# Kernel tuning notes

Hardware: AMD Instinct MI355X
Metric: run time of the kernel (lower is better)

The kernel has to match this reference:

```python
import jax, jax.numpy as jnp
import numpy as np

VOCAB, EMBED, CTX, HID = 32000, 512, 512, 1024
BATCH, MAX_LEN, START = 32, 64, 1


def setup_inputs() -> dict:
    key = jax.random.key(0)
    ks = jax.random.split(key, 12)
    s_emb = 1.0 / np.sqrt(EMBED)
    s_h = 1.0 / np.sqrt(HID)
    inp = {
        "context": jax.random.normal(ks[0], (BATCH, 1, CTX), jnp.float32),
        "max_len": MAX_LEN,
        "emb": jax.random.normal(ks[1], (VOCAB, EMBED), jnp.float32) * s_emb,
        "W_ih0": jax.random.normal(ks[2], (4 * HID, EMBED + CTX), jnp.float32) * s_h,
        "W_hh0": jax.random.normal(ks[3], (4 * HID, HID), jnp.float32) * s_h,
        "b_ih0": jax.random.normal(ks[4], (4 * HID,), jnp.float32) * s_h,
        "b_hh0": jax.random.normal(ks[5], (4 * HID,), jnp.float32) * s_h,
        "W_ih1": jax.random.normal(ks[6], (4 * HID, HID), jnp.float32) * s_h,
        "W_hh1": jax.random.normal(ks[7], (4 * HID, HID), jnp.float32) * s_h,
        "b_ih1": jax.random.normal(ks[8], (4 * HID,), jnp.float32) * s_h,
        "b_hh1": jax.random.normal(ks[9], (4 * HID,), jnp.float32) * s_h,
        "W_lin": jax.random.normal(ks[10], (VOCAB, HID), jnp.float32) * s_h,
        "b_lin": jax.random.normal(ks[11], (VOCAB,), jnp.float32) * s_h,
    }
    return inp


def _lstm_cell(x, h, c, W_ih, W_hh, b_ih, b_hh):
    # PyTorch LSTM gate order: i, f, g, o
    g = x @ W_ih.T + b_ih + h @ W_hh.T + b_hh  # (B, 4H)
    i, f, gg, o = jnp.split(g, 4, axis=-1)
    i, f, o = jax.nn.sigmoid(i), jax.nn.sigmoid(f), jax.nn.sigmoid(o)
    c_new = f * c + i * jnp.tanh(gg)
    h_new = o * jnp.tanh(c_new)
    return h_new, c_new


def reference(context, max_len, emb, W_ih0, W_hh0, b_ih0, b_hh0,
              W_ih1, W_hh1, b_ih1, b_hh1, W_lin, b_lin):
    B = context.shape[0]
    ctx = context[:, 0, :]  # (B, CTX)
    H = W_hh0.shape[1]
    x0 = jnp.full((B,), START, dtype=jnp.int32)
    zeros = jnp.zeros((B, H), jnp.float32)

    def step(carry, _):
        x, h0, c0, h1, c1 = carry
        ex = emb[x]                                   # (B, E) embedding lookup
        inp = jnp.concatenate([ex, ctx], axis=-1)      # (B, E+CTX)
        h0, c0 = _lstm_cell(inp, h0, c0, W_ih0, W_hh0, b_ih0, b_hh0)
        h1, c1 = _lstm_cell(h0, h1, c1, W_ih1, W_hh1, b_ih1, b_hh1)
        probs = jax.nn.softmax(h1 @ W_lin.T + b_lin, axis=-1)  # (B, V)
        x_next = jax.lax.stop_gradient(jnp.argmax(probs, axis=-1).astype(jnp.int32))
        return (x_next, h0, c0, h1, c1), probs

    _, probs_seq = jax.lax.scan(step, (x0, zeros, zeros, zeros, zeros), None, length=max_len)
    return jnp.transpose(probs_seq, (1, 0, 2))  # (B, max_len, V)
```

## Files before the change

### kernel.cpp

```cpp
#include <hip/hip_runtime.h>
#include <math.h>

#define B 32
#define E 512
#define CTXD 512
#define H 1024
#define G4 4096
#define V 32000
#define T 64
#define LDW 1024
#define START_TOK 1

#define OFF_GCTX   0L
#define OFF_H0     131072L
#define OFF_C0     163840L
#define OFF_H1     196608L
#define OFF_C1     229376L
#define OFF_PART0  262144L
#define OFF_PART1  1048576L
#define OFF_BSUM1  2097152L
#define OFF_SUMS   2101248L
#define OFF_AMAX   2103296L

__device__ __forceinline__ void gemm_tile(
    const float* __restrict__ W, int wcol, int j0, int xcol, int klen, int tid,
    const float* const* srow,
    float (&Wt)[64][129], float (&Xs)[32][64], float (&acc)[2][8])
{
  const int jj = tid & 63;
  const int bg = tid >> 6;
  for (int kc = 0; kc < klen; kc += 64) {
#pragma unroll
    for (int i = 0; i < 8; i++) {
      int fi  = tid + (i << 8);
      int row = fi >> 4;
      int c4  = (fi & 15) << 2;
      const float4 w4 = *(const float4*)(W + (long)(j0 + row) * LDW + (wcol + kc + c4));
      Wt[c4 + 0][row] = w4.x;
      Wt[c4 + 1][row] = w4.y;
      Wt[c4 + 2][row] = w4.z;
      Wt[c4 + 3][row] = w4.w;
    }
#pragma unroll
    for (int i = 0; i < 2; i++) {
      int fi = tid + (i << 8);
      int b  = fi >> 4;
      int c4 = (fi & 15) << 2;
      *(float4*)&Xs[b][c4] = *(const float4*)(srow[b] + xcol + kc + c4);
    }
    __syncthreads();
#pragma unroll 4
    for (int k = 0; k < 64; k += 4) {
      float wa0 = Wt[k + 0][jj],      wa1 = Wt[k + 1][jj];
      float wa2 = Wt[k + 2][jj],      wa3 = Wt[k + 3][jj];
      float wb0 = Wt[k + 0][jj + 64], wb1 = Wt[k + 1][jj + 64];
      float wb2 = Wt[k + 2][jj + 64], wb3 = Wt[k + 3][jj + 64];
#pragma unroll
      for (int g = 0; g < 8; g++) {
        const float4 xv = *(const float4*)&Xs[bg + (g << 2)][k];
        float a0 = acc[0][g], a1 = acc[1][g];
        a0 = fmaf(wa0, xv.x, a0); a0 = fmaf(wa1, xv.y, a0);
        a0 = fmaf(wa2, xv.z, a0); a0 = fmaf(wa3, xv.w, a0);
        a1 = fmaf(wb0, xv.x, a1); a1 = fmaf(wb1, xv.y, a1);
        a1 = fmaf(wb2, xv.z, a1); a1 = fmaf(wb3, xv.w, a1);
        acc[0][g] = a0; acc[1][g] = a1;
      }
    }
    __syncthreads();
  }
}

__global__ void init_kernel(float* __restrict__ ws,
                            const float* __restrict__ bih1,
                            const float* __restrict__ bhh1)
{
  int i = blockIdx.x * 256 + threadIdx.x;
  for (int k = i; k < 131072; k += 65536) ws[OFF_H0 + k] = 0.f;
  if (i < 4096) ws[OFF_BSUM1 + i] = bih1[i] + bhh1[i];
  if (i < 2048) ws[OFF_SUMS + i] = 0.f;
  if (i < 4096) ws[OFF_AMAX + i] = 0.f;
}

__global__ void gctx_kernel(float* __restrict__ ws,
                            const float* __restrict__ ctx,
                            const float* __restrict__ Wih0,
                            const float* __restrict__ bih0,
                            const float* __restrict__ bhh0)
{
  __shared__ float Wt[64][129];
  __shared__ float Xs[32][64];
  __shared__ const float* srow[32];
  const int tid = threadIdx.x;
  const int j0  = blockIdx.x * 128;
  if (tid < 32) srow[tid] = ctx + tid * CTXD;
  __syncthreads();
  float acc[2][8] = {};
  gemm_tile(Wih0, E, j0, 0, CTXD, tid, srow, Wt, Xs, acc);
  const int jj = tid & 63;
  const int bg = tid >> 6;
  const float bsA = bih0[j0 + jj]      + bhh0[j0 + jj];
  const float bsB = bih0[j0 + jj + 64] + bhh0[j0 + jj + 64];
#pragma unroll
  for (int g = 0; g < 8; g++) {
    int b = bg + (g << 2);
    float* o = ws + OFF_GCTX + (long)b * G4 + j0;
    o[jj]      = acc[0][g] + bsA;
    o[jj + 64] = acc[1][g] + bsB;
  }
}

__global__ void lstm_gemm(int layer, int t,
                          const float* __restrict__ Wih,
                          const float* __restrict__ Whh,
                          const float* __restrict__ emb,
                          float* __restrict__ ws)
{
  __shared__ float Wt[64][129];
  __shared__ float Xs[32][64];
  __shared__ const float* srow[32];
  const int tid = threadIdx.x;
  const int c   = blockIdx.y;
  const int j0  = blockIdx.x * 128;

  const float* W;
  int wcol, xcol;
  if (layer == 0) {
    if (c < 2) { W = Wih; wcol = c * 256; xcol = wcol; }
    else       { W = Whh; wcol = (c - 2) * 256; xcol = wcol; }
  } else {
    if (c < 4) { W = Wih; wcol = c * 256; xcol = wcol; }
    else       { W = Whh; wcol = (c - 4) * 256; xcol = wcol; }
  }
  if (tid < 32) {
    const float* r;
    if (layer == 0 && c < 2) {
      int tok;
      if (t == 0) tok = START_TOK;
      else {
        unsigned long long p = ((const unsigned long long*)(ws + OFF_AMAX))[(long)(t - 1) * B + tid];
        tok = (int)(0xFFFFFFFFu - (unsigned)(p & 0xFFFFFFFFull));
      }
      r = emb + (long)tok * E;
    } else if (layer == 0) {
      r = ws + OFF_H0 + (long)tid * H;
    } else {
      r = ws + (c < 4 ? OFF_H0 : OFF_H1) + (long)tid * H;
    }
    srow[tid] = r;
  }
  __syncthreads();

  float acc[2][8] = {};
  gemm_tile(W, wcol, j0, xcol, 256, tid, srow, Wt, Xs, acc);

  const int jj = tid & 63;
  const int bg = tid >> 6;
  float* part = ws + (layer == 0 ? OFF_PART0 : OFF_PART1) + (long)c * B * G4;
#pragma unroll
  for (int g = 0; g < 8; g++) {
    int b = bg + (g << 2);
    float* o = part + (long)b * G4 + j0;
    o[jj]      = acc[0][g];
    o[jj + 64] = acc[1][g];
  }
}

__global__ void cell0_kernel(float* __restrict__ ws)
{
  int idx = blockIdx.x * 256 + threadIdx.x;
  int b = idx >> 10, h = idx & 1023;
  const float* gc = ws + OFF_GCTX + (long)b * G4;
  float gi = gc[h], gf = gc[h + 1024], gg = gc[h + 2048], go = gc[h + 3072];
#pragma unroll
  for (int c = 0; c < 6; c++) {
    const float* p = ws + OFF_PART0 + ((long)c * B + b) * G4;
    gi += p[h]; gf += p[h + 1024]; gg += p[h + 2048]; go += p[h + 3072];
  }
  float i_ = 1.f / (1.f + expf(-gi));
  float f_ = 1.f / (1.f + expf(-gf));
  float o_ = 1.f / (1.f + expf(-go));
  float g_ = tanhf(gg);
  float cn = f_ * ws[OFF_C0 + idx] + i_ * g_;
  ws[OFF_C0 + idx] = cn;
  ws[OFF_H0 + idx] = o_ * tanhf(cn);
}

__global__ void cell1_kernel(float* __restrict__ ws)
{
  int idx = blockIdx.x * 256 + threadIdx.x;
  int b = idx >> 10, h = idx & 1023;
  const float* bs = ws + OFF_BSUM1;
  float gi = bs[h], gf = bs[h + 1024], gg = bs[h + 2048], go = bs[h + 3072];
#pragma unroll
  for (int c = 0; c < 8; c++) {
    const float* p = ws + OFF_PART1 + ((long)c * B + b) * G4;
    gi += p[h]; gf += p[h + 1024]; gg += p[h + 2048]; go += p[h + 3072];
  }
  float i_ = 1.f / (1.f + expf(-gi));
  float f_ = 1.f / (1.f + expf(-gf));
  float o_ = 1.f / (1.f + expf(-go));
  float g_ = tanhf(gg);
  float cn = f_ * ws[OFF_C1 + idx] + i_ * g_;
  ws[OFF_C1 + idx] = cn;
  ws[OFF_H1 + idx] = o_ * tanhf(cn);
}

__global__ void logits_kernel(float* __restrict__ ws,
                              const float* __restrict__ Wlin,
                              const float* __restrict__ blin,
                              float* __restrict__ out, int t)
{
  __shared__ float Wt[64][129];
  __shared__ float Xs[32][64];
  __shared__ const float* srow[32];
  __shared__ float ssum[32];
  __shared__ unsigned long long smax[32];
  const int tid = threadIdx.x;
  const int j0  = blockIdx.x * 128;
  if (tid < 32) {
    srow[tid] = ws + OFF_H1 + (long)tid * H;
    ssum[tid] = 0.f;
    smax[tid] = 0ull;
  }
  __syncthreads();

  float acc[2][8] = {};
  gemm_tile(Wlin, 0, j0, 0, H, tid, srow, Wt, Xs, acc);

  const int jj = tid & 63;
  const int bg = tid >> 6;
  const float bl0 = blin[j0 + jj];
  const float bl1 = blin[j0 + jj + 64];
#pragma unroll
  for (int g = 0; g < 8; g++) {
    int b = bg + (g << 2);
    float e0 = expf(acc[0][g] + bl0);
    float e1 = expf(acc[1][g] + bl1);
    long obase = ((long)b * T + t) * (long)V + j0;
    out[obase + jj]      = e0;
    out[obase + jj + 64] = e1;
    atomicAdd(&ssum[b], e0 + e1);
    unsigned long long p0 = ((unsigned long long)__float_as_uint(e0) << 32) |
                            (unsigned long long)(0xFFFFFFFFu - (unsigned)(j0 + jj));
    unsigned long long p1 = ((unsigned long long)__float_as_uint(e1) << 32) |
                            (unsigned long long)(0xFFFFFFFFu - (unsigned)(j0 + jj + 64));
    atomicMax(&smax[b], p0 > p1 ? p0 : p1);
  }
  __syncthreads();
  if (tid < 32) {
    atomicAdd(ws + OFF_SUMS + (long)t * B + tid, ssum[tid]);
    atomicMax((unsigned long long*)(ws + OFF_AMAX) + (long)t * B + tid, smax[tid]);
  }
}

__global__ void norm_kernel(float* __restrict__ out, const float* __restrict__ ws, int t)
{
  int fi = blockIdx.x * 256 + threadIdx.x;
  int b  = fi / 8000;
  int v4 = (fi - b * 8000) << 2;
  float rs = 1.f / ws[OFF_SUMS + (long)t * B + b];
  float4* p = (float4*)(out + ((long)b * T + t) * (long)V + v4);
  float4 x = *p;
  x.x *= rs; x.y *= rs; x.z *= rs; x.w *= rs;
  *p = x;
}

extern "C" void kernel_launch(void* const* d_in, const int* in_sizes, int n_in,
                              void* d_out, int out_size, void* d_ws, size_t ws_size,
                              hipStream_t stream)
{
  const float* context = (const float*)d_in[0];
  const float* emb  = (const float*)d_in[2];
  const float* Wih0 = (const float*)d_in[3];
  const float* Whh0 = (const float*)d_in[4];
  const float* bih0 = (const float*)d_in[5];
  const float* bhh0 = (const float*)d_in[6];
  const float* Wih1 = (const float*)d_in[7];
  const float* Whh1 = (const float*)d_in[8];
  const float* bih1 = (const float*)d_in[9];
  const float* bhh1 = (const float*)d_in[10];
  const float* Wlin = (const float*)d_in[11];
  const float* blin = (const float*)d_in[12];
  float* out = (float*)d_out;
  float* ws  = (float*)d_ws;

  init_kernel<<<256, 256, 0, stream>>>(ws, bih1, bhh1);
  gctx_kernel<<<32, 256, 0, stream>>>(ws, context, Wih0, bih0, bhh0);

  for (int t = 0; t < T; t++) {
    lstm_gemm<<<dim3(32, 6), 256, 0, stream>>>(0, t, Wih0, Whh0, emb, ws);
    cell0_kernel<<<128, 256, 0, stream>>>(ws);
    lstm_gemm<<<dim3(32, 8), 256, 0, stream>>>(1, t, Wih1, Whh1, emb, ws);
    cell1_kernel<<<128, 256, 0, stream>>>(ws);
    logits_kernel<<<250, 256, 0, stream>>>(ws, Wlin, blin, out, t);
    norm_kernel<<<1000, 256, 0, stream>>>(out, ws, t);
  }
}
```

Before: 10.24 ms.

## Double-buffer GEMM tiles via direct global-to-LDS loads and defer normalization

The shared GEMM tile is replaced by a 64-column version that stages weights and activations straight into LDS with global_load_lds, using an XOR swizzle and double buffering so the next tile loads while the current one computes. Grids are doubled to keep parallelism with the smaller tiles. The logits kernel now reduces sum and argmax with wavefront shuffles instead of LDS atomics. The 64 per-step normalization launches are replaced by one pass at the end. Risks are the narrow tile cutting weight reuse per block and the final pass rereading the whole output at once.

```diff
diff --git a/kernel.cpp b/kernel.cpp
--- a/kernel.cpp
+++ b/kernel.cpp
@@ -22,48 +22,71 @@
 #define OFF_SUMS   2101248L
 #define OFF_AMAX   2103296L
 
-__device__ __forceinline__ void gemm_tile(
-    const float* __restrict__ W, int wcol, int j0, int xcol, int klen, int tid,
-    const float* const* srow,
-    float (&Wt)[64][129], float (&Xs)[32][64], float (&acc)[2][8])
-{
-  const int jj = tid & 63;
-  const int bg = tid >> 6;
-  for (int kc = 0; kc < klen; kc += 64) {
-#pragma unroll
-    for (int i = 0; i < 8; i++) {
-      int fi  = tid + (i << 8);
-      int row = fi >> 4;
-      int c4  = (fi & 15) << 2;
-      const float4 w4 = *(const float4*)(W + (long)(j0 + row) * LDW + (wcol + kc + c4));
-      Wt[c4 + 0][row] = w4.x;
-      Wt[c4 + 1][row] = w4.y;
-      Wt[c4 + 2][row] = w4.z;
-      Wt[c4 + 3][row] = w4.w;
-    }
-#pragma unroll
-    for (int i = 0; i < 2; i++) {
-      int fi = tid + (i << 8);
-      int b  = fi >> 4;
-      int c4 = (fi & 15) << 2;
-      *(float4*)&Xs[b][c4] = *(const float4*)(srow[b] + xcol + kc + c4);
-    }
-    __syncthreads();
-#pragma unroll 4
-    for (int k = 0; k < 64; k += 4) {
-      float wa0 = Wt[k + 0][jj],      wa1 = Wt[k + 1][jj];
-      float wa2 = Wt[k + 2][jj],      wa3 = Wt[k + 3][jj];
-      float wb0 = Wt[k + 0][jj + 64], wb1 = Wt[k + 1][jj + 64];
-      float wb2 = Wt[k + 2][jj + 64], wb3 = Wt[k + 3][jj + 64];
+struct Smem {
+  float4 Wb[2][1024];
+  float4 Xb[2][512];
+  const float* srow[B];
+};
+
+__device__ __forceinline__ void gload16(const float* g, void* l)
+{
+  __builtin_amdgcn_global_load_lds(
+      (const __attribute__((address_space(1))) void*)g,
+      (__attribute__((address_space(3))) void*)l,
+      16, 0, 0);
+}
+
+__device__ __forceinline__ void gemm64(
+    const float* __restrict__ W, int wcol, int j0, int xcol, int klen,
+    int tid, Smem& sm, float (&acc)[8])
+{
+  const int jj  = tid & 63;
+  const int bg8 = (tid >> 6) << 3;
+  const int swz = jj & 7;
+
+  const float* wsrc[4];
+#pragma unroll
+  for (int i = 0; i < 4; i++) {
+    int r = (tid >> 4) + (i << 4);
+    wsrc[i] = W + (long)(j0 + r) * LDW
+                + (wcol + (((tid & 15) ^ (r & 7)) << 2));
+  }
+  const float* xsrc[2];
+#pragma unroll
+  for (int i = 0; i < 2; i++) {
+    int L = tid + (i << 8);
+    xsrc[i] = sm.srow[L >> 4] + xcol + ((L & 15) << 2);
+  }
+
+  auto STAGE = [&](int buf, int kc) {
+#pragma unroll
+    for (int i = 0; i < 4; i++)
+      gload16(wsrc[i] + kc, &sm.Wb[buf][tid + (i << 8)]);
+#pragma unroll
+    for (int i = 0; i < 2; i++)
+      gload16(xsrc[i] + kc, &sm.Xb[buf][tid + (i << 8)]);
+  };
+
+  const int nt = klen >> 6;
+  STAGE(0, 0);
+  __syncthreads();
+#pragma unroll 1
+  for (int t = 0; t < nt; t++) {
+    const int cur = t & 1;
+    if (t + 1 < nt) STAGE(cur ^ 1, (t + 1) << 6);
+
+    const float4* wrow = &sm.Wb[cur][jj << 4];
+    const float4* xrow = &sm.Xb[cur][bg8 << 4];
+#pragma unroll
+    for (int kq = 0; kq < 16; kq++) {
+      const float4 w4 = wrow[kq ^ swz];
 #pragma unroll
       for (int g = 0; g < 8; g++) {
-        const float4 xv = *(const float4*)&Xs[bg + (g << 2)][k];
-        float a0 = acc[0][g], a1 = acc[1][g];
-        a0 = fmaf(wa0, xv.x, a0); a0 = fmaf(wa1, xv.y, a0);
-        a0 = fmaf(wa2, xv.z, a0); a0 = fmaf(wa3, xv.w, a0);
-        a1 = fmaf(wb0, xv.x, a1); a1 = fmaf(wb1, xv.y, a1);
-        a1 = fmaf(wb2, xv.z, a1); a1 = fmaf(wb3, xv.w, a1);
-        acc[0][g] = a0; acc[1][g] = a1;
+        const float4 xv = xrow[(g << 4) + kq];
+        acc[g] = fmaf(w4.x, xv.x, acc[g]);
+        acc[g] = fmaf(w4.y, xv.y, acc[g]);
+        acc[g] = fmaf(w4.z, xv.z, acc[g]);
+        acc[g] = fmaf(w4.w, xv.w, acc[g]);
       }
     }
     __syncthreads();
@@ -81,46 +104,40 @@
   if (i < 4096) ws[OFF_AMAX + i] = 0.f;
 }
 
-__global__ void gctx_kernel(float* __restrict__ ws,
-                            const float* __restrict__ ctx,
-                            const float* __restrict__ Wih0,
-                            const float* __restrict__ bih0,
-                            const float* __restrict__ bhh0)
-{
-  __shared__ float Wt[64][129];
-  __shared__ float Xs[32][64];
-  __shared__ const float* srow[32];
+__global__ __launch_bounds__(256)
+void gctx_kernel(float* __restrict__ ws,
+                 const float* __restrict__ ctx,
+                 const float* __restrict__ Wih0,
+                 const float* __restrict__ bih0,
+                 const float* __restrict__ bhh0)
+{
+  __shared__ Smem sm;
   const int tid = threadIdx.x;
-  const int j0  = blockIdx.x * 128;
-  if (tid < 32) srow[tid] = ctx + tid * CTXD;
+  const int j0  = blockIdx.x * 64;
+  if (tid < B) sm.srow[tid] = ctx + tid * CTXD;
   __syncthreads();
-  float acc[2][8] = {};
-  gemm_tile(Wih0, E, j0, 0, CTXD, tid, srow, Wt, Xs, acc);
-  const int jj = tid & 63;
-  const int bg = tid >> 6;
-  const float bsA = bih0[j0 + jj]      + bhh0[j0 + jj];
-  const float bsB = bih0[j0 + jj + 64] + bhh0[j0 + jj + 64];
-#pragma unroll
-  for (int g = 0; g < 8; g++) {
-    int b = bg + (g << 2);
-    float* o = ws + OFF_GCTX + (long)b * G4 + j0;
-    o[jj]      = acc[0][g] + bsA;
-    o[jj + 64] = acc[1][g] + bsB;
-  }
-}
-
-__global__ void lstm_gemm(int layer, int t,
-                          const float* __restrict__ Wih,
-                          const float* __restrict__ Whh,
-                          const float* __restrict__ emb,
-                          float* __restrict__ ws)
-{
-  __shared__ float Wt[64][129];
-  __shared__ float Xs[32][64];
-  __shared__ const float* srow[32];
+
+  float acc[8] = {};
+  gemm64(Wih0, E, j0, 0, CTXD, tid, sm, acc);
+
+  const int jj = tid & 63, bg8 = (tid >> 6) << 3;
+  const float bs = bih0[j0 + jj] + bhh0[j0 + jj];
+#pragma unroll
+  for (int g = 0; g < 8; g++)
+    ws[OFF_GCTX + (long)(bg8 + g) * G4 + j0 + jj] = acc[g] + bs;
+}
+
+__global__ __launch_bounds__(256)
+void lstm_gemm(int layer, int t,
+               const float* __restrict__ Wih,
+               const float* __restrict__ Whh,
+               const float* __restrict__ emb,
+               float* __restrict__ ws)
+{
+  __shared__ Smem sm;
   const int tid = threadIdx.x;
   const int c   = blockIdx.y;
-  const int j0  = blockIdx.x * 128;
+  const int j0  = blockIdx.x * 64;
 
   const float* W;
   int wcol, xcol;
@@ -131,13 +148,14 @@
     if (c < 4) { W = Wih; wcol = c * 256; xcol = wcol; }
     else       { W = Whh; wcol = (c - 4) * 256; xcol = wcol; }
   }
-  if (tid < 32) {
+  if (tid < B) {
     const float* r;
     if (layer == 0 && c < 2) {
       int tok;
       if (t == 0) tok = START_TOK;
       else {
-        unsigned long long p = ((const unsigned long long*)(ws + OFF_AMAX))[(long)(t - 1) * B + tid];
+        unsigned long long p =
+            ((const unsigned long long*)(ws + OFF_AMAX))[(long)(t - 1) * B + tid];
         tok = (int)(0xFFFFFFFFu - (unsigned)(p & 0xFFFFFFFFull));
       }
       r = emb + (long)tok * E;
@@ -146,23 +164,18 @@
     } else {
       r = ws + (c < 4 ? OFF_H0 : OFF_H1) + (long)tid * H;
     }
-    srow[tid] = r;
+    sm.srow[tid] = r;
   }
   __syncthreads();
 
-  float acc[2][8] = {};
-  gemm_tile(W, wcol, j0, xcol, 256, tid, srow, Wt, Xs, acc);
-
-  const int jj = tid & 63;
-  const int bg = tid >> 6;
+  float acc[8] = {};
+  gemm64(W, wcol, j0, xcol, 256, tid, sm, acc);
+
+  const int jj = tid & 63, bg8 = (tid >> 6) << 3;
   float* part = ws + (layer == 0 ? OFF_PART0 : OFF_PART1) + (long)c * B * G4;
 #pragma unroll
-  for (int g = 0; g < 8; g++) {
-    int b = bg + (g << 2);
-    float* o = part + (long)b * G4 + j0;
-    o[jj]      = acc[0][g];
-    o[jj + 64] = acc[1][g];
-  }
+  for (int g = 0; g < 8; g++)
+    part[(long)(bg8 + g) * G4 + j0 + jj] = acc[g];
 }
 
 __global__ void cell0_kernel(float* __restrict__ ws)
@@ -205,61 +218,66 @@
   ws[OFF_H1 + idx] = o_ * tanhf(cn);
 }
 
-__global__ void logits_kernel(float* __restrict__ ws,
-                              const float* __restrict__ Wlin,
-                              const float* __restrict__ blin,
-                              float* __restrict__ out, int t)
-{
-  __shared__ float Wt[64][129];
-  __shared__ float Xs[32][64];
-  __shared__ const float* srow[32];
-  __shared__ float ssum[32];
-  __shared__ unsigned long long smax[32];
+__global__ __launch_bounds__(256)
+void logits_kernel(float* __restrict__ ws,
+                   const float* __restrict__ Wlin,
+                   const float* __restrict__ blin,
+                   float* __restrict__ out, int t)
+{
+  __shared__ Smem sm;
   const int tid = threadIdx.x;
-  const int j0  = blockIdx.x * 128;
-  if (tid < 32) {
-    srow[tid] = ws + OFF_H1 + (long)tid * H;
-    ssum[tid] = 0.f;
-    smax[tid] = 0ull;
-  }
+  const int j0  = blockIdx.x * 64;
+  if (tid < B) sm.srow[tid] = ws + OFF_H1 + (long)tid * H;
   __syncthreads();
 
-  float acc[2][8] = {};
-  gemm_tile(Wlin, 0, j0, 0, H, tid, srow, Wt, Xs, acc);
-
-  const int jj = tid & 63;
-  const int bg = tid >> 6;
-  const float bl0 = blin[j0 + jj];
-  const float bl1 = blin[j0 + jj + 64];
+  float acc[8] = {};
+  gemm64(Wlin, 0, j0, 0, H, tid, sm, acc);
+
+  const int jj = tid & 63, bg8 = (tid >> 6) << 3;
+  const int j  = j0 + jj;
+  const float bl = blin[j];
+
+  float ev[8];
 #pragma unroll
   for (int g = 0; g < 8; g++) {
-    int b = bg + (g << 2);
-    float e0 = expf(acc[0][g] + bl0);
-    float e1 = expf(acc[1][g] + bl1);
-    long obase = ((long)b * T + t) * (long)V + j0;
-    out[obase + jj]      = e0;
-    out[obase + jj + 64] = e1;
-    atomicAdd(&ssum[b], e0 + e1);
-    unsigned long long p0 = ((unsigned long long)__float_as_uint(e0) << 32) |
-                            (unsigned long long)(0xFFFFFFFFu - (unsigned)(j0 + jj));
-    unsigned long long p1 = ((unsigned long long)__float_as_uint(e1) << 32) |
-                            (unsigned long long)(0xFFFFFFFFu - (unsigned)(j0 + jj + 64));
-    atomicMax(&smax[b], p0 > p1 ? p0 : p1);
-  }
-  __syncthreads();
-  if (tid < 32) {
-    atomicAdd(ws + OFF_SUMS + (long)t * B + tid, ssum[tid]);
-    atomicMax((unsigned long long*)(ws + OFF_AMAX) + (long)t * B + tid, smax[tid]);
-  }
-}
-
-__global__ void norm_kernel(float* __restrict__ out, const float* __restrict__ ws, int t)
-{
-  int fi = blockIdx.x * 256 + threadIdx.x;
-  int b  = fi / 8000;
-  int v4 = (fi - b * 8000) << 2;
+    ev[g] = expf(acc[g] + bl);
+    out[((long)(bg8 + g) * T + t) * (long)V + j] = ev[g];
+  }
+
+  float rs[8];
+  unsigned long long rm[8];
+#pragma unroll
+  for (int g = 0; g < 8; g++) {
+    rs[g] = ev[g];
+    rm[g] = ((unsigned long long)__float_as_uint(ev[g]) << 32)
+          | (unsigned long long)(0xFFFFFFFFu - (unsigned)j);
+  }
+#pragma unroll
+  for (int off = 32; off > 0; off >>= 1) {
+#pragma unroll
+    for (int g = 0; g < 8; g++) {
+      rs[g] += __shfl_xor(rs[g], off);
+      unsigned long long o = __shfl_xor(rm[g], off);
+      rm[g] = o > rm[g] ? o : rm[g];
+    }
+  }
+#pragma unroll
+  for (int g = 0; g < 8; g++) {
+    if (jj == g) {
+      atomicAdd(ws + OFF_SUMS + (long)t * B + (bg8 + g), rs[g]);
+      atomicMax((unsigned long long*)(ws + OFF_AMAX) + (long)t * B + (bg8 + g), rm[g]);
+    }
+  }
+}
+
+__global__ void norm_all(float* __restrict__ out, const float* __restrict__ ws)
+{
+  int i  = blockIdx.x * 256 + threadIdx.x;
+  int bt = i / 8000;
+  int v4 = (i - bt * 8000) << 2;
+  int b  = bt >> 6, t = bt & 63;
   float rs = 1.f / ws[OFF_SUMS + (long)t * B + b];
-  float4* p = (float4*)(out + ((long)b * T + t) * (long)V + v4);
+  float4* p = (float4*)(out + (long)bt * V + v4);
   float4 x = *p;
   x.x *= rs; x.y *= rs; x.z *= rs; x.w *= rs;
   *p = x;
@@ -285,14 +303,14 @@
   float* ws  = (float*)d_ws;
 
   init_kernel<<<256, 256, 0, stream>>>(ws, bih1, bhh1);
-  gctx_kernel<<<32, 256, 0, stream>>>(ws, context, Wih0, bih0, bhh0);
+  gctx_kernel<<<64, 256, 0, stream>>>(ws, context, Wih0, bih0, bhh0);
 
   for (int t = 0; t < T; t++) {
-    lstm_gemm<<<dim3(32, 6), 256, 0, stream>>>(0, t, Wih0, Whh0, emb, ws);
+    lstm_gemm<<<dim3(64, 6), 256, 0, stream>>>(0, t, Wih0, Whh0, emb, ws);
     cell0_kernel<<<128, 256, 0, stream>>>(ws);
-    lstm_gemm<<<dim3(32, 8), 256, 0, stream>>>(1, t, Wih1, Whh1, emb, ws);
+    lstm_gemm<<<dim3(64, 8), 256, 0, stream>>>(1, t, Wih1, Whh1, emb, ws);
     cell1_kernel<<<128, 256, 0, stream>>>(ws);
-    logits_kernel<<<250, 256, 0, stream>>>(ws, Wlin, blin, out, t);
-    norm_kernel<<<1000, 256, 0, stream>>>(out, ws, t);
-  }
-}
+    logits_kernel<<<500, 256, 0, stream>>>(ws, Wlin, blin, out, t);
+  }
+  norm_all<<<64000, 256, 0, stream>>>(out, ws);
+}
```

After: 9.915 ms. 3.2% less time.
